# Optimization experiments

Measured on AMD Instinct MI355X. Metric: run time of the kernel, lower is better.

Reference implementation:

```python
import jax, jax.numpy as jnp
import numpy as np

HID = 2048; H = 16; QLR = 1536; KVLR = 512
DN = 128; DR = 64; DV = 128; DQ = DN + DR  # 192
B = 2; S = 2048
THETA = 10000.0; EPS = 1e-6


def rms_norm(x, w, eps=EPS):
    x32 = x.astype(jnp.float32)
    var = jnp.mean(x32 * x32, axis=-1, keepdims=True)
    return (w * (x32 * jax.lax.rsqrt(var + eps))).astype(x.dtype)


def rotate_half(x):
    x1, x2 = jnp.split(x, 2, axis=-1)
    return jnp.concatenate((-x2, x1), axis=-1)


def rope_tables(seq_len, dim, base=THETA):
    inv_freq = 1.0 / (base ** (jnp.arange(0, dim, 2, dtype=jnp.float32) / dim))
    t = jnp.arange(seq_len, dtype=jnp.float32)
    freqs = jnp.outer(t, inv_freq)            # [S, dim/2]
    emb = jnp.concatenate((freqs, freqs), -1)  # [S, dim]
    return jnp.cos(emb), jnp.sin(emb)


def setup_inputs() -> dict:
    key = jax.random.key(0)
    ks = jax.random.split(key, 8)
    sd = lambda fan_in: 1.0 / np.sqrt(fan_in)
    return {
        "hidden_states": jax.random.normal(ks[0], (B, S, HID), jnp.float32),
        "w_qa": jax.random.normal(ks[1], (QLR, HID), jnp.float32) * sd(HID),
        "q_a_ln_w": jnp.ones((QLR,), jnp.float32),
        "w_qb": jax.random.normal(ks[2], (H * DQ, QLR), jnp.float32) * sd(QLR),
        "w_kva": jax.random.normal(ks[3], (KVLR + DR, HID), jnp.float32) * sd(HID),
        "kv_a_ln_w": jnp.ones((KVLR,), jnp.float32),
        "w_kvb": jax.random.normal(ks[4], (H * (DN + DV), KVLR), jnp.float32) * sd(KVLR),
        "w_o": jax.random.normal(ks[5], (HID, H * DV), jnp.float32) * sd(H * DV),
    }


def reference(hidden_states, w_qa, q_a_ln_w, w_qb, w_kva, kv_a_ln_w, w_kvb, w_o):
    b, s, _ = hidden_states.shape
    scale = DQ ** -0.5
    cos, sin = rope_tables(s, DR)  # [S, DR] each

    # Q path: low-rank down-proj -> RMSNorm -> up-proj
    cq = rms_norm(hidden_states @ w_qa.T, q_a_ln_w)            # [B,S,QLR]
    q = (cq @ w_qb.T).reshape(b, s, H, DQ).transpose(0, 2, 1, 3)  # [B,H,S,DQ]
    q_nope, q_pe = q[..., :DN], q[..., DN:]
    q_pe = q_pe * cos + rotate_half(q_pe) * sin

    # KV path: joint compressed kv + shared rope key
    ckv = hidden_states @ w_kva.T                               # [B,S,KVLR+DR]
    k_pe = ckv[..., KVLR:].reshape(b, s, 1, DR).transpose(0, 2, 1, 3)  # [B,1,S,DR]
    k_pe = k_pe * cos + rotate_half(k_pe) * sin
    ckv_l = rms_norm(ckv[..., :KVLR], kv_a_ln_w)                # [B,S,KVLR]
    kv = (ckv_l @ w_kvb.T).reshape(b, s, H, DN + DV).transpose(0, 2, 1, 3)
    k_nope, v = kv[..., :DN], kv[..., DN:]                      # [B,H,S,DN],[B,H,S,DV]

    q_full = jnp.concatenate([q_nope, q_pe], axis=-1)           # [B,H,S,DQ]
    k_full = jnp.concatenate(
        [k_nope, jnp.broadcast_to(k_pe, (b, H, s, DR))], axis=-1)

    scores = jnp.einsum('bhqd,bhkd->bhqk', q_full, k_full) * scale
    causal = jnp.triu(jnp.ones((s, s), dtype=bool), k=1)
    scores = jnp.where(causal, -jnp.inf, scores)
    attn = jax.nn.softmax(scores.astype(jnp.float32), axis=-1).astype(q_full.dtype)

    out = jnp.einsum('bhqk,bhkd->bhqd', attn, v)                # [B,H,S,DV]
    out = out.transpose(0, 2, 1, 3).reshape(b, s, H * DV)
    return out @ w_o.T
```

## Files before the change

kernel.cpp:

```cpp
#include <hip/hip_runtime.h>
#include <stdint.h>
#include <stddef.h>

typedef unsigned short u16;
typedef short s16x8 __attribute__((ext_vector_type(8)));
typedef unsigned short u16x4 __attribute__((ext_vector_type(4)));
typedef unsigned short u16x8 __attribute__((ext_vector_type(8)));
typedef float f32x4 __attribute__((ext_vector_type(4)));

__device__ __forceinline__ u16 f2b(float f) {
  uint32_t u = __builtin_bit_cast(uint32_t, f);
  uint32_t r = u + 0x7fffu + ((u >> 16) & 1u);
  return (u16)(r >> 16);
}
__device__ __forceinline__ float b2f(u16 h) {
  uint32_t u = ((uint32_t)h) << 16;
  return __builtin_bit_cast(float, u);
}
__device__ __forceinline__ void gl_lds16(const void* g, void* l) {
  __builtin_amdgcn_global_load_lds((const __attribute__((address_space(1))) void*)g,
                                   (__attribute__((address_space(3))) void*)l,
                                   16, 0, 0);
}

__global__ __launch_bounds__(256) void cast_k(const float* __restrict__ in,
                                              u16* __restrict__ out, int n4) {
  int i = blockIdx.x * 256 + threadIdx.x;
  if (i >= n4) return;
  float4 v = ((const float4*)in)[i];
  u16x4 o; o[0]=f2b(v.x); o[1]=f2b(v.y); o[2]=f2b(v.z); o[3]=f2b(v.w);
  ((u16x4*)out)[i] = o;
}

__global__ __launch_bounds__(256) void cast_pad_k(const float* __restrict__ in,
                                                  u16* __restrict__ out,
                                                  int Kd, int nvalid, int n4) {
  int i = blockIdx.x * 256 + threadIdx.x;
  if (i >= n4) return;
  int row = (i << 2) / Kd;
  u16x4 o;
  if (row < nvalid) {
    float4 v = ((const float4*)in)[i];
    o[0]=f2b(v.x); o[1]=f2b(v.y); o[2]=f2b(v.z); o[3]=f2b(v.w);
  } else {
    o[0]=0; o[1]=0; o[2]=0; o[3]=0;
  }
  ((u16x4*)out)[i] = o;
}

template<int OUT_BF16>
__global__ __launch_bounds__(256) void gemm_bt(const u16* __restrict__ A,
                                               const u16* __restrict__ B,
                                               void* __restrict__ Cv,
                                               int M, int N, int K) {
  __shared__ u16 As[128 * 32];
  __shared__ u16 Bs[128 * 32];
  const int t = threadIdx.x;
  const int w = t >> 6, l = t & 63;
  const int nb = N >> 7;
  const int bm = (blockIdx.x / nb) << 7;
  const int bn = (blockIdx.x % nb) << 7;
  const int wr = (w >> 1) << 6;
  const int wc = (w & 1) << 6;

  f32x4 acc[4][4];
  #pragma unroll
  for (int i = 0; i < 4; i++)
    #pragma unroll
    for (int j = 0; j < 4; j++) acc[i][j] = (f32x4){0.f, 0.f, 0.f, 0.f};

  const u16* ga = A + (size_t)(bm + w * 32 + (l >> 2)) * K + ((l & 3) * 8);
  const u16* gb = B + (size_t)(bn + w * 32 + (l >> 2)) * K + ((l & 3) * 8);
  u16* la0 = &As[(w * 32) * 32];
  u16* la1 = &As[(w * 32 + 16) * 32];
  u16* lb0 = &Bs[(w * 32) * 32];
  u16* lb1 = &Bs[(w * 32 + 16) * 32];

  for (int k0 = 0; k0 < K; k0 += 32) {
    __syncthreads();
    gl_lds16(ga, la0);
    gl_lds16(ga + (size_t)16 * K, la1);
    gl_lds16(gb, lb0);
    gl_lds16(gb + (size_t)16 * K, lb1);
    ga += 32; gb += 32;
    __syncthreads();

    s16x8 af[4], bf[4];
    #pragma unroll
    for (int i = 0; i < 4; i++) {
      af[i] = *(const s16x8*)&As[(wr + i * 16 + (l & 15)) * 32 + (l >> 4) * 8];
      bf[i] = *(const s16x8*)&Bs[(wc + i * 16 + (l & 15)) * 32 + (l >> 4) * 8];
    }
    #pragma unroll
    for (int mi = 0; mi < 4; mi++)
      #pragma unroll
      for (int ni = 0; ni < 4; ni++)
        acc[mi][ni] = __builtin_amdgcn_mfma_f32_16x16x32_bf16(af[mi], bf[ni], acc[mi][ni], 0, 0, 0);
  }

  #pragma unroll
  for (int mi = 0; mi < 4; mi++)
    #pragma unroll
    for (int ni = 0; ni < 4; ni++) {
      int row0 = bm + wr + mi * 16 + ((l >> 4) << 2);
      int col  = bn + wc + ni * 16 + (l & 15);
      #pragma unroll
      for (int r = 0; r < 4; r++) {
        float v = acc[mi][ni][r];
        if (OUT_BF16) ((u16*)Cv)[(size_t)(row0 + r) * N + col] = f2b(v);
        else          ((float*)Cv)[(size_t)(row0 + r) * N + col] = v;
      }
    }
}

__global__ __launch_bounds__(256) void rmsnorm_k(const float* __restrict__ X,
                                                 const float* __restrict__ W,
                                                 u16* __restrict__ Y, int ldx, int D) {
  const int row = blockIdx.x;
  const float* x = X + (size_t)row * ldx;
  const int t = threadIdx.x;
  float ss = 0.f;
  for (int i = t; i < (D >> 2); i += 256) {
    float4 v = ((const float4*)x)[i];
    ss += v.x * v.x + v.y * v.y + v.z * v.z + v.w * v.w;
  }
  #pragma unroll
  for (int off = 32; off > 0; off >>= 1) ss += __shfl_xor(ss, off);
  __shared__ float red[4];
  if ((t & 63) == 0) red[t >> 6] = ss;
  __syncthreads();
  float tot = red[0] + red[1] + red[2] + red[3];
  float r = rsqrtf(tot / (float)D + 1e-6f);
  u16* y = Y + (size_t)row * D;
  for (int i = t; i < (D >> 2); i += 256) {
    float4 v = ((const float4*)x)[i];
    float4 g = ((const float4*)W)[i];
    u16x4 o;
    o[0] = f2b(v.x * r * g.x); o[1] = f2b(v.y * r * g.y);
    o[2] = f2b(v.z * r * g.z); o[3] = f2b(v.w * r * g.w);
    ((u16x4*)y)[i] = o;
  }
}

__global__ __launch_bounds__(256) void rope_kpe_k(const float* __restrict__ CKV,
                                                  u16* __restrict__ Kpe) {
  int idx = blockIdx.x * 256 + threadIdx.x;
  if (idx >= 4096 * 32) return;
  int d = idx & 31;
  int m = idx >> 5;
  int s = m & 2047;
  float inv = expf(-(float)(2 * d) * (9.210340371976184f / 64.0f));
  float ang = (float)s * inv;
  float sn, c;
  sincosf(ang, &sn, &c);
  float x1 = CKV[(size_t)m * 640 + 512 + d];
  float x2 = CKV[(size_t)m * 640 + 544 + d];
  Kpe[m * 64 + d]      = f2b(x1 * c - x2 * sn);
  Kpe[m * 64 + 32 + d] = f2b(x2 * c + x1 * sn);
}

__global__ __launch_bounds__(256) void rope_q_k(u16* __restrict__ Qb) {
  int idx = blockIdx.x * 256 + threadIdx.x;
  if (idx >= 4096 * 16 * 32) return;
  int d = idx & 31;
  int h = (idx >> 5) & 15;
  int m = idx >> 9;
  int s = m & 2047;
  float inv = expf(-(float)(2 * d) * (9.210340371976184f / 64.0f));
  float ang = (float)s * inv;
  float sn, c;
  sincosf(ang, &sn, &c);
  size_t base = (size_t)m * 3072 + h * 192 + 128 + d;
  float x1 = b2f(Qb[base]);
  float x2 = b2f(Qb[base + 32]);
  Qb[base]      = f2b(x1 * c - x2 * sn);
  Qb[base + 32] = f2b(x2 * c + x1 * sn);
}

__global__ __launch_bounds__(256) void vt_k(const u16* __restrict__ KV,
                                            u16* __restrict__ VT) {
  __shared__ u16 L[64][72];
  const int t = threadIdx.x;
  const int s_t = blockIdx.x & 31;
  const int d_t = (blockIdx.x >> 5) & 1;
  const int bh  = blockIdx.x >> 6;
  const int h = bh & 15, b = bh >> 4;
  const size_t bS = (size_t)b * 2048;
  const int s0 = s_t << 6, d0 = d_t << 6;

  #pragma unroll
  for (int i = 0; i < 2; i++) {
    int rs = (t >> 3) + i * 32;
    int ch = t & 7;
    u16x8 v = *(const u16x8*)&KV[(bS + s0 + rs) * 4096 + h * 256 + 128 + d0 + ch * 8];
    *(u16x8*)&L[rs][ch * 8] = v;
  }
  __syncthreads();
  #pragma unroll
  for (int i = 0; i < 2; i++) {
    int rd = (t >> 3) + i * 32;
    int ch = t & 7;
    u16x8 o;
    #pragma unroll
    for (int j = 0; j < 8; j++) o[j] = L[ch * 8 + j][rd];
    *(u16x8*)&VT[((size_t)bh * 128 + d0 + rd) * 2048 + s0 + ch * 8] = o;
  }
}

__global__ __launch_bounds__(256, 3) void attn2_k(const u16* __restrict__ Q,
                                                  const u16* __restrict__ KV,
                                                  const u16* __restrict__ Kpe,
                                                  const u16* __restrict__ VT,
                                                  u16* __restrict__ O) {
  const float SCALE = 0.07216878364870322f;
  const int t = threadIdx.x, w = t >> 6, l = t & 63;
  const int bh = blockIdx.x & 31;
  const int qt = 31 - (blockIdx.x >> 5);
  const int h = bh & 15, b = bh >> 4;
  const int q0 = qt << 6;
  const size_t bS = (size_t)b * 2048;

  __shared__ u16 Kl[64 * 192];
  __shared__ u16 Pl[4][16][72];

  s16x8 qf[6];
  {
    const u16* qp = Q + (bS + q0 + w * 16 + (l & 15)) * 3072 + h * 192 + ((l >> 4) * 8);
    #pragma unroll
    for (int c = 0; c < 6; c++) qf[c] = *(const s16x8*)(qp + c * 32);
  }
  float m_i[4] = {-1e30f, -1e30f, -1e30f, -1e30f};
  float l_i[4] = {0.f, 0.f, 0.f, 0.f};
  f32x4 accO[8];
  #pragma unroll
  for (int i = 0; i < 8; i++) accO[i] = (f32x4){0.f, 0.f, 0.f, 0.f};

  const u16* vb = VT + (size_t)bh * 128 * 2048;
  const int ktiles = qt + 1;

  for (int kt = 0; kt < ktiles; ++kt) {
    const int k0 = kt << 6;
    __syncthreads();
    #pragma unroll
    for (int it = 0; it < 6; ++it) {
      int sl = it * 64 + l;
      int r = w * 16 + sl / 24;
      int cc = (sl % 24) ^ (r & 7);
      const u16* src = (cc < 16)
          ? KV + (bS + k0 + r) * 4096 + h * 256 + cc * 8
          : Kpe + (bS + k0 + r) * 64 + (cc - 16) * 8;
      gl_lds16(src, &Kl[w * 3072 + it * 512]);
    }
    __syncthreads();

    f32x4 sa[4];
    #pragma unroll
    for (int cf = 0; cf < 4; cf++) sa[cf] = (f32x4){0.f, 0.f, 0.f, 0.f};
    #pragma unroll
    for (int c = 0; c < 6; c++) {
      #pragma unroll
      for (int cf = 0; cf < 4; cf++) {
        int row = cf * 16 + (l & 15);
        int ch = (c * 4 + (l >> 4)) ^ (row & 7);
        s16x8 kf = *(const s16x8*)&Kl[row * 192 + ch * 8];
        sa[cf] = __builtin_amdgcn_mfma_f32_16x16x32_bf16(qf[c], kf, sa[cf], 0, 0, 0);
      }
    }

    const bool diag = (kt == qt);
    #pragma unroll
    for (int r = 0; r < 4; r++) {
      float s0 = sa[0][r] * SCALE, s1 = sa[1][r] * SCALE;
      float s2 = sa[2][r] * SCALE, s3 = sa[3][r] * SCALE;
      if (diag) {
        int qrow = q0 + w * 16 + ((l >> 4) << 2) + r;
        if (k0 +      (l & 15) > qrow) s0 = -1e30f;
        if (k0 + 16 + (l & 15) > qrow) s1 = -1e30f;
        if (k0 + 32 + (l & 15) > qrow) s2 = -1e30f;
        if (k0 + 48 + (l & 15) > qrow) s3 = -1e30f;
      }
      float mx = fmaxf(fmaxf(s0, s1), fmaxf(s2, s3));
      #pragma unroll
      for (int dd = 1; dd < 16; dd <<= 1) mx = fmaxf(mx, __shfl_xor(mx, dd));
      float mnew = fmaxf(m_i[r], mx);
      float e0 = __expf(s0 - mnew), e1 = __expf(s1 - mnew);
      float e2 = __expf(s2 - mnew), e3 = __expf(s3 - mnew);
      float sum = (e0 + e1) + (e2 + e3);
      #pragma unroll
      for (int dd = 1; dd < 16; dd <<= 1) sum += __shfl_xor(sum, dd);
      float alpha = __expf(m_i[r] - mnew);
      l_i[r] = l_i[r] * alpha + sum;
      m_i[r] = mnew;
      #pragma unroll
      for (int df = 0; df < 8; df++) accO[df][r] *= alpha;
      int prow = ((l >> 4) << 2) + r;
      Pl[w][prow][(l & 15)]      = f2b(e0);
      Pl[w][prow][16 + (l & 15)] = f2b(e1);
      Pl[w][prow][32 + (l & 15)] = f2b(e2);
      Pl[w][prow][48 + (l & 15)] = f2b(e3);
    }

    #pragma unroll
    for (int sub = 0; sub < 2; sub++) {
      s16x8 pf = *(const s16x8*)&Pl[w][l & 15][sub * 32 + (l >> 4) * 8];
      #pragma unroll
      for (int df = 0; df < 8; df++) {
        s16x8 vf = *(const s16x8*)&vb[(size_t)(df * 16 + (l & 15)) * 2048 +
                                      (k0 + sub * 32 + (l >> 4) * 8)];
        accO[df] = __builtin_amdgcn_mfma_f32_16x16x32_bf16(pf, vf, accO[df], 0, 0, 0);
      }
    }
  }

  #pragma unroll
  for (int r = 0; r < 4; r++) {
    float rl = 1.0f / l_i[r];
    #pragma unroll
    for (int df = 0; df < 8; df++) {
      float o = accO[df][r] * rl;
      O[(bS + q0 + w * 16 + ((l >> 4) << 2) + r) * 2048 + h * 128 + df * 16 + (l & 15)] = f2b(o);
    }
  }
}

extern "C" void kernel_launch(void* const* d_in, const int* in_sizes, int n_in,
                              void* d_out, int out_size, void* d_ws, size_t ws_size,
                              hipStream_t stream) {
  const float* hs    = (const float*)d_in[0];
  const float* w_qa  = (const float*)d_in[1];
  const float* q_ln  = (const float*)d_in[2];
  const float* w_qb  = (const float*)d_in[3];
  const float* w_kva = (const float*)d_in[4];
  const float* kv_ln = (const float*)d_in[5];
  const float* w_kvb = (const float*)d_in[6];
  const float* w_o   = (const float*)d_in[7];
  float* out = (float*)d_out;

  char* ws = (char*)d_ws;
  size_t off = 0;
  auto alloc = [&](size_t bytes) -> void* {
    void* p = ws + off;
    off = (off + bytes + 255) & ~(size_t)255;
    return p;
  };
  u16* Xb     = (u16*)alloc(4096ull * 2048 * 2);
  u16* Wqa    = (u16*)alloc(1536ull * 2048 * 2);
  u16* Wqb    = (u16*)alloc(3072ull * 1536 * 2);
  u16* Wkva   = (u16*)alloc(640ull * 2048 * 2);
  u16* Wkvb   = (u16*)alloc(4096ull * 512 * 2);
  u16* Wo     = (u16*)alloc(2048ull * 2048 * 2);
  float* CQraw = (float*)alloc(4096ull * 1536 * 4);
  float* CKV   = (float*)alloc(4096ull * 640 * 4);
  u16* CQn    = (u16*)alloc(4096ull * 1536 * 2);
  u16* CKVn   = (u16*)alloc(4096ull * 512 * 2);
  u16* Kpe    = (u16*)alloc(4096ull * 64 * 2);
  u16* KVb    = (u16*)alloc(4096ull * 4096 * 2);
  u16* Ob     = (u16*)alloc(4096ull * 2048 * 2);
  u16* Qb     = (u16*)CQraw;
  u16* VT     = Xb;

  cast_k<<<dim3(8388608 / 4 / 256), 256, 0, stream>>>(hs, Xb, 8388608 / 4);
  cast_k<<<dim3(3145728 / 4 / 256), 256, 0, stream>>>(w_qa, Wqa, 3145728 / 4);
  cast_k<<<dim3(4718592 / 4 / 256), 256, 0, stream>>>(w_qb, Wqb, 4718592 / 4);
  cast_pad_k<<<dim3(1310720 / 4 / 256), 256, 0, stream>>>(w_kva, Wkva, 2048, 576, 1310720 / 4);
  cast_k<<<dim3(2097152 / 4 / 256), 256, 0, stream>>>(w_kvb, Wkvb, 2097152 / 4);
  cast_k<<<dim3(4194304 / 4 / 256), 256, 0, stream>>>(w_o, Wo, 4194304 / 4);

  gemm_bt<0><<<dim3(32 * 12), 256, 0, stream>>>(Xb, Wqa, CQraw, 4096, 1536, 2048);
  gemm_bt<0><<<dim3(32 * 5), 256, 0, stream>>>(Xb, Wkva, CKV, 4096, 640, 2048);

  rmsnorm_k<<<dim3(4096), 256, 0, stream>>>(CQraw, q_ln, CQn, 1536, 1536);
  rmsnorm_k<<<dim3(4096), 256, 0, stream>>>(CKV, kv_ln, CKVn, 640, 512);
  rope_kpe_k<<<dim3(4096 * 32 / 256), 256, 0, stream>>>(CKV, Kpe);

  gemm_bt<1><<<dim3(32 * 24), 256, 0, stream>>>(CQn, Wqb, Qb, 4096, 3072, 1536);
  gemm_bt<1><<<dim3(32 * 32), 256, 0, stream>>>(CKVn, Wkvb, KVb, 4096, 4096, 512);
  rope_q_k<<<dim3(4096 * 16 * 32 / 256), 256, 0, stream>>>(Qb);

  vt_k<<<dim3(32 * 2 * 32), 256, 0, stream>>>(KVb, VT);

  attn2_k<<<dim3(32 * 32), 256, 0, stream>>>(Qb, KVb, Kpe, VT, Ob);

  gemm_bt<0><<<dim3(32 * 16), 256, 0, stream>>>(Ob, Wo, out, 4096, 2048, 2048);
}
```

Baseline: 633.5 us.

## Double-buffer attention K tiles, prefetch V, lazy softmax rescale, swizzle GEMM blocks

The attention kernel now stages the next K tile into a second LDS buffer while computing on the current one, and issues the V fragment loads before the QK MFMAs to hide global latency. The online softmax skips the per-tile cross-lane max reduction and accumulator rescale unless some row max grows by more than a threshold, and defers the row-sum shuffle reduction to the end. The GEMM block index is remapped across groups of eight so that neighbouring blocks share tiles in cache. The cost is double the LDS for K, more live registers for the V fragments, and the removal of the occupancy hint from launch bounds, which may lower occupancy. The lazy rescale also lets exponentials grow up to e^8 before renormalising.

```diff
diff --git a/kernel.cpp b/kernel.cpp
--- a/kernel.cpp
+++ b/kernel.cpp
@@ -58,8 +58,10 @@
   const int t = threadIdx.x;
   const int w = t >> 6, l = t & 63;
   const int nb = N >> 7;
-  const int bm = (blockIdx.x / nb) << 7;
-  const int bn = (blockIdx.x % nb) << 7;
+  const int cpx = gridDim.x >> 3;
+  const int swz = (blockIdx.x & 7) * cpx + (blockIdx.x >> 3);
+  const int bm = (swz / nb) << 7;
+  const int bn = (swz % nb) << 7;
   const int wr = (w >> 1) << 6;
   const int wc = (w & 1) << 6;
 
@@ -207,11 +209,11 @@
   }
 }
 
-__global__ __launch_bounds__(256, 3) void attn2_k(const u16* __restrict__ Q,
-                                                  const u16* __restrict__ KV,
-                                                  const u16* __restrict__ Kpe,
-                                                  const u16* __restrict__ VT,
-                                                  u16* __restrict__ O) {
+__global__ __launch_bounds__(256) void attn3_k(const u16* __restrict__ Q,
+                                               const u16* __restrict__ KV,
+                                               const u16* __restrict__ Kpe,
+                                               const u16* __restrict__ VT,
+                                               u16* __restrict__ O) {
   const float SCALE = 0.07216878364870322f;
   const int t = threadIdx.x, w = t >> 6, l = t & 63;
   const int bh = blockIdx.x & 31;
@@ -220,7 +222,7 @@
   const int q0 = qt << 6;
   const size_t bS = (size_t)b * 2048;
 
-  __shared__ u16 Kl[64 * 192];
+  __shared__ u16 Kl[2][64 * 192];
   __shared__ u16 Pl[4][16][72];
 
   s16x8 qf[6];
@@ -230,17 +232,15 @@
     for (int c = 0; c < 6; c++) qf[c] = *(const s16x8*)(qp + c * 32);
   }
   float m_i[4] = {-1e30f, -1e30f, -1e30f, -1e30f};
-  float l_i[4] = {0.f, 0.f, 0.f, 0.f};
+  float lp[4]  = {0.f, 0.f, 0.f, 0.f};
   f32x4 accO[8];
   #pragma unroll
   for (int i = 0; i < 8; i++) accO[i] = (f32x4){0.f, 0.f, 0.f, 0.f};
 
-  const u16* vb = VT + (size_t)bh * 128 * 2048;
+  const u16* vbp = VT + (size_t)bh * 128 * 2048;
   const int ktiles = qt + 1;
 
-  for (int kt = 0; kt < ktiles; ++kt) {
-    const int k0 = kt << 6;
-    __syncthreads();
+  auto STAGE = [&](int buf, int k0) {
     #pragma unroll
     for (int it = 0; it < 6; ++it) {
       int sl = it * 64 + l;
@@ -249,9 +249,25 @@
       const u16* src = (cc < 16)
           ? KV + (bS + k0 + r) * 4096 + h * 256 + cc * 8
           : Kpe + (bS + k0 + r) * 64 + (cc - 16) * 8;
-      gl_lds16(src, &Kl[w * 3072 + it * 512]);
-    }
-    __syncthreads();
+      gl_lds16(src, &Kl[buf][w * 3072 + it * 512]);
+    }
+  };
+
+  STAGE(0, 0);
+  __syncthreads();
+
+  int cur = 0;
+  for (int kt = 0; kt < ktiles; ++kt) {
+    const int k0 = kt << 6;
+    if (kt + 1 < ktiles) STAGE(cur ^ 1, k0 + 64);
+
+    s16x8 va[8], vb[8];
+    #pragma unroll
+    for (int df = 0; df < 8; df++)
+      va[df] = *(const s16x8*)&vbp[(size_t)(df * 16 + (l & 15)) * 2048 + k0 + (l >> 4) * 8];
+    #pragma unroll
+    for (int df = 0; df < 8; df++)
+      vb[df] = *(const s16x8*)&vbp[(size_t)(df * 16 + (l & 15)) * 2048 + k0 + 32 + (l >> 4) * 8];
 
     f32x4 sa[4];
     #pragma unroll
@@ -262,37 +278,51 @@
       for (int cf = 0; cf < 4; cf++) {
         int row = cf * 16 + (l & 15);
         int ch = (c * 4 + (l >> 4)) ^ (row & 7);
-        s16x8 kf = *(const s16x8*)&Kl[row * 192 + ch * 8];
+        s16x8 kf = *(const s16x8*)&Kl[cur][row * 192 + ch * 8];
         sa[cf] = __builtin_amdgcn_mfma_f32_16x16x32_bf16(qf[c], kf, sa[cf], 0, 0, 0);
       }
     }
 
     const bool diag = (kt == qt);
     #pragma unroll
+    for (int cf = 0; cf < 4; cf++)
+      #pragma unroll
+      for (int r = 0; r < 4; r++) {
+        float s = sa[cf][r] * SCALE;
+        if (diag) {
+          int qrow = q0 + w * 16 + ((l >> 4) << 2) + r;
+          if (k0 + cf * 16 + (l & 15) > qrow) s = -1e30f;
+        }
+        sa[cf][r] = s;
+      }
+
+    float lm[4];
+    #pragma unroll
+    for (int r = 0; r < 4; r++)
+      lm[r] = fmaxf(fmaxf(sa[0][r], sa[1][r]), fmaxf(sa[2][r], sa[3][r]));
+    bool safe = (lm[0] <= m_i[0] + 8.f) && (lm[1] <= m_i[1] + 8.f) &&
+                (lm[2] <= m_i[2] + 8.f) && (lm[3] <= m_i[3] + 8.f);
+    if (!__all(safe)) {
+      #pragma unroll
+      for (int r = 0; r < 4; r++) {
+        float mx = lm[r];
+        #pragma unroll
+        for (int dd = 1; dd < 16; dd <<= 1) mx = fmaxf(mx, __shfl_xor(mx, dd));
+        float mnew = fmaxf(m_i[r], mx);
+        float alpha = __expf(m_i[r] - mnew);
+        m_i[r] = mnew;
+        lp[r] *= alpha;
+        #pragma unroll
+        for (int df = 0; df < 8; df++) accO[df][r] *= alpha;
+      }
+    }
+    #pragma unroll
     for (int r = 0; r < 4; r++) {
-      float s0 = sa[0][r] * SCALE, s1 = sa[1][r] * SCALE;
-      float s2 = sa[2][r] * SCALE, s3 = sa[3][r] * SCALE;
-      if (diag) {
-        int qrow = q0 + w * 16 + ((l >> 4) << 2) + r;
-        if (k0 +      (l & 15) > qrow) s0 = -1e30f;
-        if (k0 + 16 + (l & 15) > qrow) s1 = -1e30f;
-        if (k0 + 32 + (l & 15) > qrow) s2 = -1e30f;
-        if (k0 + 48 + (l & 15) > qrow) s3 = -1e30f;
-      }
-      float mx = fmaxf(fmaxf(s0, s1), fmaxf(s2, s3));
-      #pragma unroll
-      for (int dd = 1; dd < 16; dd <<= 1) mx = fmaxf(mx, __shfl_xor(mx, dd));
-      float mnew = fmaxf(m_i[r], mx);
-      float e0 = __expf(s0 - mnew), e1 = __expf(s1 - mnew);
-      float e2 = __expf(s2 - mnew), e3 = __expf(s3 - mnew);
-      float sum = (e0 + e1) + (e2 + e3);
-      #pragma unroll
-      for (int dd = 1; dd < 16; dd <<= 1) sum += __shfl_xor(sum, dd);
-      float alpha = __expf(m_i[r] - mnew);
-      l_i[r] = l_i[r] * alpha + sum;
-      m_i[r] = mnew;
-      #pragma unroll
-      for (int df = 0; df < 8; df++) accO[df][r] *= alpha;
+      float e0 = __expf(sa[0][r] - m_i[r]);
+      float e1 = __expf(sa[1][r] - m_i[r]);
+      float e2 = __expf(sa[2][r] - m_i[r]);
+      float e3 = __expf(sa[3][r] - m_i[r]);
+      lp[r] += (e0 + e1) + (e2 + e3);
       int prow = ((l >> 4) << 2) + r;
       Pl[w][prow][(l & 15)]      = f2b(e0);
       Pl[w][prow][16 + (l & 15)] = f2b(e1);
@@ -300,21 +330,27 @@
       Pl[w][prow][48 + (l & 15)] = f2b(e3);
     }
 
-    #pragma unroll
-    for (int sub = 0; sub < 2; sub++) {
-      s16x8 pf = *(const s16x8*)&Pl[w][l & 15][sub * 32 + (l >> 4) * 8];
-      #pragma unroll
-      for (int df = 0; df < 8; df++) {
-        s16x8 vf = *(const s16x8*)&vb[(size_t)(df * 16 + (l & 15)) * 2048 +
-                                      (k0 + sub * 32 + (l >> 4) * 8)];
-        accO[df] = __builtin_amdgcn_mfma_f32_16x16x32_bf16(pf, vf, accO[df], 0, 0, 0);
-      }
-    }
+    {
+      s16x8 pf0 = *(const s16x8*)&Pl[w][l & 15][(l >> 4) * 8];
+      #pragma unroll
+      for (int df = 0; df < 8; df++)
+        accO[df] = __builtin_amdgcn_mfma_f32_16x16x32_bf16(pf0, va[df], accO[df], 0, 0, 0);
+      s16x8 pf1 = *(const s16x8*)&Pl[w][l & 15][32 + (l >> 4) * 8];
+      #pragma unroll
+      for (int df = 0; df < 8; df++)
+        accO[df] = __builtin_amdgcn_mfma_f32_16x16x32_bf16(pf1, vb[df], accO[df], 0, 0, 0);
+    }
+
+    __syncthreads();
+    cur ^= 1;
   }
 
   #pragma unroll
   for (int r = 0; r < 4; r++) {
-    float rl = 1.0f / l_i[r];
+    float s = lp[r];
+    #pragma unroll
+    for (int dd = 1; dd < 16; dd <<= 1) s += __shfl_xor(s, dd);
+    float rl = 1.0f / s;
     #pragma unroll
     for (int df = 0; df < 8; df++) {
       float o = accO[df][r] * rl;
@@ -379,7 +415,7 @@
 
   vt_k<<<dim3(32 * 2 * 32), 256, 0, stream>>>(KVb, VT);
 
-  attn2_k<<<dim3(32 * 32), 256, 0, stream>>>(Qb, KVb, Kpe, VT, Ob);
+  attn3_k<<<dim3(32 * 32), 256, 0, stream>>>(Qb, KVb, Kpe, VT, Ob);
 
   gemm_bt<0><<<dim3(32 * 16), 256, 0, stream>>>(Ob, Wo, out, 4096, 2048, 2048);
 }
```

Measured after the change: 561.6 us. 1.13x faster.
